# Kernel optimization log

Hardware: AMD Instinct MI355X
Metric: run time of the kernel (lower is better)

Reference implementation:

```python
import jax, jax.numpy as jnp
import numpy as np

EPS_NORM = 1e-7   # Normalize module eps (added to norm)
EPS_COS = 1e-8    # torch F.cosine_similarity default eps (clamped denom)


def _normalize(x):
    # Normalize(power=2): x / (||x||_2 + 1e-7), norm over dim 1
    n = jnp.sqrt(jnp.sum(x * x, axis=1, keepdims=True))
    return x / (n + EPS_NORM)


def _cos_sim_matrix(f):
    # pairwise cosine similarity, matching torch cosine_similarity semantics:
    # (f_i . f_j) / max(||f_i|| * ||f_j||, eps)
    n = jnp.linalg.norm(f, axis=1)            # [N]
    denom = jnp.maximum(n[:, None] * n[None, :], EPS_COS)
    return (f @ f.T) / denom                   # [N, N]


def setup_inputs() -> dict:
    key = jax.random.key(0)
    kq, kk = jax.random.split(key)
    N, D = 4096, 1024
    feat_q = jax.random.normal(kq, (N, D), dtype=jnp.float32)
    feat_k = jax.random.normal(kk, (N, D), dtype=jnp.float32)
    return {"feat_q": feat_q, "feat_k": feat_k}


def reference(feat_q, feat_k):
    q = _normalize(feat_q)
    k = jax.lax.stop_gradient(_normalize(feat_k))  # feat_k.detach()
    Sq = _cos_sim_matrix(q)   # [N, N]
    Sk = _cos_sim_matrix(k)   # [N, N]
    N = feat_q.shape[0]
    off_diag = ~jnp.eye(N, dtype=bool)
    diff2 = (Sq - Sk) ** 2
    # mean over the N*(N-1) off-diagonal (i != j) pairs
    loss = jnp.sum(jnp.where(off_diag, diff2, 0.0)) / (N * (N - 1))
    return loss
```

## Files before the change

kernel.cpp:

```cpp
#include <hip/hip_runtime.h>
#include <stdint.h>

#define N_ROWS 4096
#define DIMS   1024
#define BM 128
#define BK 128
#define TG 16
#define NTRI 136
#define KSPLIT 4
#define KCHUNK 1024
#define NITER  (KCHUNK / BK)

typedef __attribute__((ext_vector_type(2))) long longx2;
typedef __attribute__((ext_vector_type(4))) float f32x4;

__device__ __forceinline__ unsigned short f2bf(float f) {
  union { float f; unsigned int u; } c; c.f = f;
  unsigned int u = c.u;
  return (unsigned short)((u + 0x7fffu + ((u >> 16) & 1u)) >> 16);
}
__device__ __forceinline__ float bf2f(unsigned short v) {
  union { float f; unsigned int u; } c; c.u = ((unsigned int)v) << 16;
  return c.f;
}
__device__ __forceinline__ unsigned int pk4_fp8(float a, float b, float c, float d) {
  int v = __builtin_amdgcn_cvt_pk_fp8_f32(a, b, 0, false);
  v = __builtin_amdgcn_cvt_pk_fp8_f32(c, d, v, true);
  return (unsigned int)v;
}
__device__ __forceinline__ void async_cp16(const unsigned char* g, void* lds) {
  __builtin_amdgcn_global_load_lds(
      (const __attribute__((address_space(1))) void*)g,
      (__attribute__((address_space(3))) void*)lds, 16, 0, 0);
}

__global__ __launch_bounds__(256) void rownorm_kernel(
    const float* __restrict__ fq, const float* __restrict__ fk,
    float* __restrict__ invq, float* __restrict__ invk, float* __restrict__ out) {
  if (blockIdx.x == 0 && blockIdx.y == 0 && threadIdx.x == 0) out[0] = 0.0f;
  const int w = threadIdx.x >> 6, lane = threadIdx.x & 63;
  const int row = blockIdx.x * 4 + w;
  const float* src = blockIdx.y ? fk : fq;
  float* dst = blockIdx.y ? invk : invq;
  const float4* s4 = (const float4*)(src + (size_t)row * DIMS);
  float ss = 0.0f;
  #pragma unroll
  for (int s = 0; s < 4; ++s) {
    float4 v = s4[lane + 64 * s];
    ss += v.x * v.x + v.y * v.y + v.z * v.z + v.w * v.w;
  }
  #pragma unroll
  for (int off = 32; off > 0; off >>= 1) ss += __shfl_xor(ss, off);
  if (lane == 0) dst[row] = 1.0f / sqrtf(ss);
}

__global__ __launch_bounds__(256) void transpose_scale_kernel(
    const float* __restrict__ fq, const float* __restrict__ fk,
    const float* __restrict__ invq, const float* __restrict__ invk,
    unsigned char* __restrict__ Mt) {
  __shared__ unsigned short tile[64][260];
  const int i0 = blockIdx.x * 256;
  const int a0 = blockIdx.y * 64;
  const int w = threadIdx.x >> 6, lane = threadIdx.x & 63;
  const float* src;
  const float* inv;
  int acol;
  if (a0 < DIMS) { src = fq; inv = invq; acol = a0 + lane; }
  else           { src = fk; inv = invk; acol = a0 - DIMS + lane; }

  for (int c0 = 0; c0 < 64; c0 += 4) {
    ushort4 v;
    unsigned short* vp = (unsigned short*)&v;
    #pragma unroll
    for (int c = 0; c < 4; ++c) {
      const int i = i0 + w * 64 + c0 + c;
      vp[c] = f2bf(src[(size_t)i * DIMS + acol] * inv[i]);
    }
    *(ushort4*)&tile[lane][w * 64 + c0] = v;
  }
  __syncthreads();
  const int il = (lane * 4) & 127;
  const int blk = (i0 + lane * 4) >> 7;
  const int q = (il >> 3) & 3, s0 = (il >> 5) & 1, s1 = (il >> 6) & 1;
  const int pos = q * 32 + s1 * 16 + s0 * 8 + (il & 7);
  #pragma unroll
  for (int r = 0; r < 16; ++r) {
    const int al = w * 16 + r;
    ushort4 v = *(const ushort4*)&tile[al][lane * 4];
    const unsigned int p8 = pk4_fp8(bf2f(v.x), bf2f(v.y), bf2f(v.z), bf2f(v.w));
    *(unsigned int*)(Mt + (size_t)(a0 + al) * N_ROWS + blk * 128 + pos) = p8;
  }
}

__global__ __launch_bounds__(256, 2) void gram_partial_kernel(
    const unsigned char* __restrict__ Mt, unsigned short* __restrict__ Gp) {
  __shared__ __align__(16) char smem[2][2 * BM * BK];

  const int t = blockIdx.x >> 2;
  const int kc = blockIdx.x & 3;
  int I = 0, rem = t;
  while (rem >= (TG - I)) { rem -= (TG - I); ++I; }
  const int J = I + rem;

  const int tid = threadIdx.x, w = tid >> 6, lane = tid & 63;

  const int isB = w >> 1;
  const int rblk = isB ? J : I;
  const int rl = lane >> 3;
  const int cl = (lane & 7) ^ rl;
  const bool skipStage = (isB && I == J);
  const unsigned char* gsrc0 =
      Mt + (size_t)(rblk * BM + (w & 1) * 64 + rl) * N_ROWS + kc * KCHUNK + cl * 16;
  const int ldsOff = isB * 16384 + (w & 1) * 8192;
  const int bOff = (I == J) ? 0 : 16384;

  const int wr = w >> 1, wc = w & 1;
  const int ml = lane & 15, quad = lane >> 4;
  const int ar0 = wr * 64, bc0 = wc * 64;

  f32x4 acc[4][4] = {};

  if (!skipStage) {
    #pragma unroll
    for (int s = 0; s < 8; ++s)
      async_cp16(gsrc0 + (size_t)s * 8 * N_ROWS, smem[0] + ldsOff + s * 1024);
  }

  #pragma unroll
  for (int it = 0; it < NITER; ++it) {
    __syncthreads();
    if (it + 1 < NITER && !skipStage) {
      const unsigned char* g = gsrc0 + (it + 1) * BK;
      char* dst = smem[(it + 1) & 1] + ldsOff;
      #pragma unroll
      for (int s = 0; s < 8; ++s)
        async_cp16(g + (size_t)s * 8 * N_ROWS, dst + s * 1024);
    }
    const char* buf = smem[it & 1];
    longx2 a[4][2], b[4][2];
    #pragma unroll
    for (int i = 0; i < 4; ++i) {
      const int ra = (ar0 + i * 16 + ml) * BK;
      const int rb = (bc0 + i * 16 + ml) * BK;
      #pragma unroll
      for (int s1 = 0; s1 < 2; ++s1) {
        const int slot = ((quad * 2 + s1) ^ (ml & 7)) * 16;
        a[i][s1] = *(const longx2*)(buf + ra + slot);
        b[i][s1] = *(const longx2*)(buf + bOff + rb + slot);
      }
    }
    #pragma unroll
    for (int s1 = 0; s1 < 2; ++s1)
      #pragma unroll
      for (int h = 0; h < 2; ++h)
        #pragma unroll
        for (int i = 0; i < 4; ++i)
          #pragma unroll
          for (int j = 0; j < 4; ++j)
            acc[i][j] = __builtin_amdgcn_mfma_f32_16x16x32_fp8_fp8(
                a[i][s1][h], b[j][s1][h], acc[i][j], 0, 0, 0);
  }

  unsigned short* slab = Gp + (size_t)blockIdx.x * (BM * BM) + w * 4096;
  #pragma unroll
  for (int i = 0; i < 4; ++i)
    #pragma unroll
    for (int j = 0; j < 4; ++j) {
      ushort4 o;
      o.x = f2bf(acc[i][j][0]); o.y = f2bf(acc[i][j][1]);
      o.z = f2bf(acc[i][j][2]); o.w = f2bf(acc[i][j][3]);
      *(ushort4*)(slab + (i * 4 + j) * 256 + lane * 4) = o;
    }
}

__global__ __launch_bounds__(256) void square_reduce_kernel(
    const unsigned short* __restrict__ Gp, float* __restrict__ out) {
  __shared__ float wsum[4];
  const int t = blockIdx.x >> 3;
  const int seg = blockIdx.x & 7;
  int I = 0, rem = t;
  while (rem >= (TG - I)) { rem -= (TG - I); ++I; }
  const int J = I + rem;

  const unsigned short* base =
      Gp + (size_t)t * (KSPLIT * BM * BM) + seg * 2048 + threadIdx.x * 8;
  float s[8] = {0, 0, 0, 0, 0, 0, 0, 0};
  #pragma unroll
  for (int kc = 0; kc < KSPLIT; ++kc) {
    const ushort4 v0 = *(const ushort4*)(base + kc * (BM * BM));
    const ushort4 v1 = *(const ushort4*)(base + kc * (BM * BM) + 4);
    s[0] += bf2f(v0.x); s[1] += bf2f(v0.y); s[2] += bf2f(v0.z); s[3] += bf2f(v0.w);
    s[4] += bf2f(v1.x); s[5] += bf2f(v1.y); s[6] += bf2f(v1.z); s[7] += bf2f(v1.w);
  }
  float local = 0.0f;
  #pragma unroll
  for (int x = 0; x < 8; ++x) local += s[x] * s[x];

  const float sgn = ((I < 8) == (J < 8)) ? 1.0f : -1.0f;
  local *= (I == J ? 1.0f : 2.0f) * sgn;

  #pragma unroll
  for (int off = 32; off > 0; off >>= 1) local += __shfl_xor(local, off);
  const int w = threadIdx.x >> 6, lane = threadIdx.x & 63;
  if (lane == 0) wsum[w] = local;
  __syncthreads();
  if (threadIdx.x == 0) {
    const float ts = wsum[0] + wsum[1] + wsum[2] + wsum[3];
    atomicAdd(out, ts * (1.0f / 16773120.0f));
  }
}

extern "C" void kernel_launch(void* const* d_in, const int* in_sizes, int n_in,
                              void* d_out, int out_size, void* d_ws, size_t ws_size,
                              hipStream_t stream) {
  const float* fq = (const float*)d_in[0];
  const float* fk = (const float*)d_in[1];
  float* invq = (float*)d_ws;
  float* invk = invq + N_ROWS;
  unsigned char* Mt = (unsigned char*)d_ws + 32768;
  unsigned short* Gp = (unsigned short*)(Mt + (size_t)2048 * N_ROWS);
  float* out = (float*)d_out;

  rownorm_kernel<<<dim3(N_ROWS / 4, 2), 256, 0, stream>>>(fq, fk, invq, invk, out);
  transpose_scale_kernel<<<dim3(16, 32), 256, 0, stream>>>(fq, fk, invq, invk, Mt);
  gram_partial_kernel<<<NTRI * KSPLIT, 256, 0, stream>>>(Mt, Gp);
  square_reduce_kernel<<<NTRI * 8, 256, 0, stream>>>(Gp, out);
}
```

Baseline: 116.8 us.

## Fuse rownorm with transpose and fold the split-K reduction into the gram kernel

Merges the row-norm and transpose/fp8-quantize kernels into one prep kernel, where each block handles 16 rows, computes their inverse norms in LDS and writes fp8 directly, dropping the bf16 intermediate. The separate square-reduce kernel is removed: the last of the K-split blocks for each tile, found through an atomic counter, sums the partials and does the squared reduction. Block-to-job mapping is also interleaved across K-chunks. This cuts two launches and one global round-trip. The cost is a less coalesced prep access pattern (16-row tiles, byte-wise LDS writes) and a serial tail reduction in the last block of each tile.

Result: slower. 183.2 us (+56.8%).

```diff
diff --git a/kernel.cpp b/kernel.cpp
--- a/kernel.cpp
+++ b/kernel.cpp
@@ -10,6 +10,7 @@
 #define KSPLIT 4
 #define KCHUNK 1024
 #define NITER  (KCHUNK / BK)
+#define NJOBS  (NTRI * KSPLIT)
 
 typedef __attribute__((ext_vector_type(2))) long longx2;
 typedef __attribute__((ext_vector_type(4))) float f32x4;
@@ -34,70 +35,73 @@
       (__attribute__((address_space(3))) void*)lds, 16, 0, 0);
 }
 
-__global__ __launch_bounds__(256) void rownorm_kernel(
+__global__ __launch_bounds__(256) void prep_kernel(
     const float* __restrict__ fq, const float* __restrict__ fk,
-    float* __restrict__ invq, float* __restrict__ invk, float* __restrict__ out) {
-  if (blockIdx.x == 0 && blockIdx.y == 0 && threadIdx.x == 0) out[0] = 0.0f;
+    unsigned char* __restrict__ Mt, float* __restrict__ out,
+    int* __restrict__ counters) {
+  if (blockIdx.x == 0 && blockIdx.y == 0) {
+    if (threadIdx.x == 0) out[0] = 0.0f;
+    if (threadIdx.x < NTRI) counters[threadIdx.x] = 0;
+  }
+  const int i0 = blockIdx.x * 16;
+  const float* src = blockIdx.y ? fk : fq;
+  const int aBase = blockIdx.y ? DIMS : 0;
+
+  __shared__ float invLds[16];
+  __shared__ unsigned char tile8[2][64 * 20];
+
   const int w = threadIdx.x >> 6, lane = threadIdx.x & 63;
-  const int row = blockIdx.x * 4 + w;
-  const float* src = blockIdx.y ? fk : fq;
-  float* dst = blockIdx.y ? invk : invq;
-  const float4* s4 = (const float4*)(src + (size_t)row * DIMS);
-  float ss = 0.0f;
-  #pragma unroll
-  for (int s = 0; s < 4; ++s) {
-    float4 v = s4[lane + 64 * s];
-    ss += v.x * v.x + v.y * v.y + v.z * v.z + v.w * v.w;
-  }
-  #pragma unroll
-  for (int off = 32; off > 0; off >>= 1) ss += __shfl_xor(ss, off);
-  if (lane == 0) dst[row] = 1.0f / sqrtf(ss);
-}
-
-__global__ __launch_bounds__(256) void transpose_scale_kernel(
-    const float* __restrict__ fq, const float* __restrict__ fk,
-    const float* __restrict__ invq, const float* __restrict__ invk,
-    unsigned char* __restrict__ Mt) {
-  __shared__ unsigned short tile[64][260];
-  const int i0 = blockIdx.x * 256;
-  const int a0 = blockIdx.y * 64;
-  const int w = threadIdx.x >> 6, lane = threadIdx.x & 63;
-  const float* src;
-  const float* inv;
-  int acol;
-  if (a0 < DIMS) { src = fq; inv = invq; acol = a0 + lane; }
-  else           { src = fk; inv = invk; acol = a0 - DIMS + lane; }
-
-  for (int c0 = 0; c0 < 64; c0 += 4) {
-    ushort4 v;
-    unsigned short* vp = (unsigned short*)&v;
-    #pragma unroll
-    for (int c = 0; c < 4; ++c) {
-      const int i = i0 + w * 64 + c0 + c;
-      vp[c] = f2bf(src[(size_t)i * DIMS + acol] * inv[i]);
-    }
-    *(ushort4*)&tile[lane][w * 64 + c0] = v;
+  #pragma unroll
+  for (int rr = 0; rr < 4; ++rr) {
+    const int r = w * 4 + rr;
+    const float4* s4 = (const float4*)(src + (size_t)(i0 + r) * DIMS);
+    float ss = 0.0f;
+    #pragma unroll
+    for (int s = 0; s < 4; ++s) {
+      float4 v = s4[lane + 64 * s];
+      ss += v.x * v.x + v.y * v.y + v.z * v.z + v.w * v.w;
+    }
+    #pragma unroll
+    for (int off = 32; off > 0; off >>= 1) ss += __shfl_xor(ss, off);
+    if (lane == 0) invLds[r] = 1.0f / sqrtf(ss);
   }
   __syncthreads();
-  const int il = (lane * 4) & 127;
-  const int blk = (i0 + lane * 4) >> 7;
-  const int q = (il >> 3) & 3, s0 = (il >> 5) & 1, s1 = (il >> 6) & 1;
-  const int pos = q * 32 + s1 * 16 + s0 * 8 + (il & 7);
-  #pragma unroll
-  for (int r = 0; r < 16; ++r) {
-    const int al = w * 16 + r;
-    ushort4 v = *(const ushort4*)&tile[al][lane * 4];
-    const unsigned int p8 = pk4_fp8(bf2f(v.x), bf2f(v.y), bf2f(v.z), bf2f(v.w));
-    *(unsigned int*)(Mt + (size_t)(a0 + al) * N_ROWS + blk * 128 + pos) = p8;
+
+  const int iloc = i0 & 127;
+  const int blk = i0 >> 7;
+  const int ti = threadIdx.x >> 4;
+  const int ta4 = (threadIdx.x & 15) * 4;
+  const int ra = threadIdx.x >> 2;
+  const int riw = threadIdx.x & 3;
+  const int il = iloc + riw * 4;
+  const int q = (il >> 3) & 3, s0b = (il >> 5) & 1, s1b = (il >> 6) & 1;
+  const int pos = q * 32 + s1b * 16 + s0b * 8 + (il & 7);
+  const float invI = invLds[ti];
+
+  for (int c = 0; c < 16; ++c) {
+    unsigned char* tb = tile8[c & 1];
+    const float4 v = *(const float4*)(src + (size_t)(i0 + ti) * DIMS + c * 64 + ta4);
+    const unsigned int p = pk4_fp8(v.x * invI, v.y * invI, v.z * invI, v.w * invI);
+    tb[(ta4 + 0) * 20 + ti] = (unsigned char)(p);
+    tb[(ta4 + 1) * 20 + ti] = (unsigned char)(p >> 8);
+    tb[(ta4 + 2) * 20 + ti] = (unsigned char)(p >> 16);
+    tb[(ta4 + 3) * 20 + ti] = (unsigned char)(p >> 24);
+    __syncthreads();
+    const unsigned int dw = *(const unsigned int*)&tb[ra * 20 + riw * 4];
+    *(unsigned int*)(Mt + (size_t)(aBase + c * 64 + ra) * N_ROWS + blk * 128 + pos) = dw;
   }
 }
 
 __global__ __launch_bounds__(256, 2) void gram_partial_kernel(
-    const unsigned char* __restrict__ Mt, unsigned short* __restrict__ Gp) {
+    const unsigned char* __restrict__ Mt, unsigned short* __restrict__ Gp,
+    int* __restrict__ counters, float* __restrict__ out) {
   __shared__ __align__(16) char smem[2][2 * BM * BK];
-
-  const int t = blockIdx.x >> 2;
-  const int kc = blockIdx.x & 3;
+  __shared__ int lastFlag;
+  __shared__ float wsum[4];
+
+  const int job = (blockIdx.x & 7) * (NJOBS / 8) + (blockIdx.x >> 3);
+  const int t = job >> 2;
+  const int kc = job & 3;
   int I = 0, rem = t;
   while (rem >= (TG - I)) { rem -= (TG - I); ++I; }
   const int J = I + rem;
@@ -161,7 +165,7 @@
                 a[i][s1][h], b[j][s1][h], acc[i][j], 0, 0, 0);
   }
 
-  unsigned short* slab = Gp + (size_t)blockIdx.x * (BM * BM) + w * 4096;
+  unsigned short* slab = Gp + (size_t)job * (BM * BM) + w * 4096;
   #pragma unroll
   for (int i = 0; i < 4; ++i)
     #pragma unroll
@@ -171,40 +175,36 @@
       o.z = f2bf(acc[i][j][2]); o.w = f2bf(acc[i][j][3]);
       *(ushort4*)(slab + (i * 4 + j) * 256 + lane * 4) = o;
     }
-}
-
-__global__ __launch_bounds__(256) void square_reduce_kernel(
-    const unsigned short* __restrict__ Gp, float* __restrict__ out) {
-  __shared__ float wsum[4];
-  const int t = blockIdx.x >> 3;
-  const int seg = blockIdx.x & 7;
-  int I = 0, rem = t;
-  while (rem >= (TG - I)) { rem -= (TG - I); ++I; }
-  const int J = I + rem;
-
-  const unsigned short* base =
-      Gp + (size_t)t * (KSPLIT * BM * BM) + seg * 2048 + threadIdx.x * 8;
-  float s[8] = {0, 0, 0, 0, 0, 0, 0, 0};
-  #pragma unroll
-  for (int kc = 0; kc < KSPLIT; ++kc) {
-    const ushort4 v0 = *(const ushort4*)(base + kc * (BM * BM));
-    const ushort4 v1 = *(const ushort4*)(base + kc * (BM * BM) + 4);
-    s[0] += bf2f(v0.x); s[1] += bf2f(v0.y); s[2] += bf2f(v0.z); s[3] += bf2f(v0.w);
-    s[4] += bf2f(v1.x); s[5] += bf2f(v1.y); s[6] += bf2f(v1.z); s[7] += bf2f(v1.w);
-  }
+
+  __threadfence();
+  if (tid == 0) lastFlag = (atomicAdd(&counters[t], 1) == KSPLIT - 1);
+  __syncthreads();
+  if (!lastFlag) return;
+  __threadfence();
+
+  const unsigned short* tb = Gp + (size_t)t * (KSPLIT * BM * BM);
   float local = 0.0f;
   #pragma unroll
-  for (int x = 0; x < 8; ++x) local += s[x] * s[x];
-
+  for (int seg = 0; seg < 8; ++seg) {
+    const unsigned short* base = tb + seg * 2048 + tid * 8;
+    float s[8] = {0, 0, 0, 0, 0, 0, 0, 0};
+    #pragma unroll
+    for (int k2 = 0; k2 < KSPLIT; ++k2) {
+      const ushort4 v0 = *(const ushort4*)(base + k2 * (BM * BM));
+      const ushort4 v1 = *(const ushort4*)(base + k2 * (BM * BM) + 4);
+      s[0] += bf2f(v0.x); s[1] += bf2f(v0.y); s[2] += bf2f(v0.z); s[3] += bf2f(v0.w);
+      s[4] += bf2f(v1.x); s[5] += bf2f(v1.y); s[6] += bf2f(v1.z); s[7] += bf2f(v1.w);
+    }
+    #pragma unroll
+    for (int x = 0; x < 8; ++x) local += s[x] * s[x];
+  }
   const float sgn = ((I < 8) == (J < 8)) ? 1.0f : -1.0f;
   local *= (I == J ? 1.0f : 2.0f) * sgn;
-
   #pragma unroll
   for (int off = 32; off > 0; off >>= 1) local += __shfl_xor(local, off);
-  const int w = threadIdx.x >> 6, lane = threadIdx.x & 63;
   if (lane == 0) wsum[w] = local;
   __syncthreads();
-  if (threadIdx.x == 0) {
+  if (tid == 0) {
     const float ts = wsum[0] + wsum[1] + wsum[2] + wsum[3];
     atomicAdd(out, ts * (1.0f / 16773120.0f));
   }
@@ -215,14 +215,11 @@
                               hipStream_t stream) {
   const float* fq = (const float*)d_in[0];
   const float* fk = (const float*)d_in[1];
-  float* invq = (float*)d_ws;
-  float* invk = invq + N_ROWS;
-  unsigned char* Mt = (unsigned char*)d_ws + 32768;
+  unsigned char* Mt = (unsigned char*)d_ws;
   unsigned short* Gp = (unsigned short*)(Mt + (size_t)2048 * N_ROWS);
+  int* counters = (int*)(Gp + (size_t)NJOBS * BM * BM);
   float* out = (float*)d_out;
 
-  rownorm_kernel<<<dim3(N_ROWS / 4, 2), 256, 0, stream>>>(fq, fk, invq, invk, out);
-  transpose_scale_kernel<<<dim3(16, 32), 256, 0, stream>>>(fq, fk, invq, invk, Mt);
-  gram_partial_kernel<<<NTRI * KSPLIT, 256, 0, stream>>>(Mt, Gp);
-  square_reduce_kernel<<<NTRI * 8, 256, 0, stream>>>(Gp, out);
-}
+  prep_kernel<<<dim3(256, 2), 256, 0, stream>>>(fq, fk, Mt, out, counters);
+  gram_partial_kernel<<<NJOBS, 256, 0, stream>>>(Mt, Gp, counters, out);
+}
```
